# Optimization experiments

Hardware: AMD Instinct MI355X
Metric: run time of the kernel (lower is better)

The kernel has to match this reference:

```python
import jax, jax.numpy as jnp
import numpy as np

NUM_HEADS = 8
T = 8  # hardcoded temporal dim in the original forward
MD = 3  # max_displacement -> 7x7 window
EPS = 1e-12  # F.normalize eps


def l2_normalize(x, axis):
    n = jnp.sqrt(jnp.sum(x * x, axis=axis, keepdims=True))
    return x / jnp.maximum(n, EPS)


def correlation_7x7(q, k):
    # q, k: [B, C, H, W]; FlowNet-style correlation, kernel_size=1, max_disp=3.
    # out[b, u, v, h, w] = sum_c q[b,c,h,w] * k[b,c,h+u-3,w+v-3] (zero padded)
    B, C, H, W = q.shape
    kp = jnp.pad(k, ((0, 0), (0, 0), (MD, MD), (MD, MD)))
    outs = []
    for dy in range(2 * MD + 1):
        for dx in range(2 * MD + 1):
            ks = kp[:, :, dy:dy + H, dx:dx + W]
            outs.append(jnp.sum(q * ks, axis=1))  # [B, H, W]
    corr = jnp.stack(outs, axis=1)  # [B, 49, H, W]
    return corr.reshape(B, 2 * MD + 1, 2 * MD + 1, H, W)


def setup_inputs() -> dict:
    key = jax.random.key(0)
    ks = jax.random.split(key, 6)
    B, N, C = 8, 8192, 256
    hd = C // NUM_HEADS
    std = 0.02
    return {
        "x": jax.random.normal(ks[0], (B, N, C), dtype=jnp.float32),
        "w_qk": jax.random.normal(ks[1], (2 * C, C), dtype=jnp.float32) * std,
        "w_corr": jax.random.normal(ks[2], (hd, 49), dtype=jnp.float32) * std,
        "b_corr": jnp.zeros((hd,), dtype=jnp.float32),
        "w_proj": jax.random.normal(ks[3], (C, C), dtype=jnp.float32) * std,
        "b_proj": jnp.zeros((C,), dtype=jnp.float32),
    }


def reference(x, w_qk, w_corr, b_corr, w_proj, b_proj):
    B, N, C = x.shape
    nh = NUM_HEADS
    hd = C // nh
    H = int(np.sqrt(N // T))
    W = H

    # qk projection (no bias): [B, N, 2C] -> q, k each [B, nh, N, hd]
    qk = jnp.einsum('bnc,dc->bnd', x, w_qk)
    qk = qk.reshape(B, N, 2, nh, hd).transpose(2, 0, 3, 1, 4)
    q, k = qk[0], qk[1]

    # 'b n (t h w) d -> (b n) t d h w'
    q = q.reshape(B * nh, T, H, W, hd).transpose(0, 1, 4, 2, 3)
    k = k.reshape(B * nh, T, H, W, hd).transpose(0, 1, 4, 2, 3)

    # temporal postfix: k[t+1], last frame repeated
    k_post = jnp.concatenate([k[:, 1:], k[:, -1:]], axis=1)

    qp = q.reshape(B * nh * T, hd, H, W)
    kp = k_post.reshape(B * nh * T, hd, H, W)
    qp = l2_normalize(qp, axis=1)
    kp = l2_normalize(kp, axis=1)

    corr = correlation_7x7(qp, kp)  # [(B nh T), 7, 7, H, W]
    # 'b u v h w -> b (h w) (u v)'
    corr = corr.transpose(0, 3, 4, 1, 2).reshape(B * nh * T, H * W, 49)

    v = jnp.einsum('bpk,dk->bpd', corr, w_corr) + b_corr  # [(B nh T), HW, hd]

    # '(b n t) (h w) d -> b n (t h w) d' then 'b h n d -> b n (h d)'
    out = v.reshape(B, nh, T * H * W, hd).transpose(0, 2, 1, 3).reshape(B, N, C)
    out = jnp.einsum('bnc,dc->bnd', out, w_proj) + b_proj
    return out
```

## Files before the change

### kernel.cpp

```cpp
#include <hip/hip_runtime.h>

typedef _Float16 half8 __attribute__((ext_vector_type(8)));
typedef _Float16 half2v __attribute__((ext_vector_type(2)));
typedef float float4v __attribute__((ext_vector_type(4)));

__device__ __forceinline__ float dot2acc(unsigned a, unsigned b, float c) {
#if __has_builtin(__builtin_amdgcn_fdot2)
  return __builtin_amdgcn_fdot2(__builtin_bit_cast(half2v, a), __builtin_bit_cast(half2v, b), c, false);
#else
  half2v ha = __builtin_bit_cast(half2v, a);
  half2v hb = __builtin_bit_cast(half2v, b);
  c += (float)ha[0] * (float)hb[0];
  c += (float)ha[1] * (float)hb[1];
  return c;
#endif
}
__device__ __forceinline__ unsigned hscale(unsigned a, float s) {
  half2v ha = __builtin_bit_cast(half2v, a);
  half2v r;
  r[0] = (_Float16)((float)ha[0] * s);
  r[1] = (_Float16)((float)ha[1] * s);
  return __builtin_bit_cast(unsigned, r);
}
__device__ __forceinline__ void gload_lds16(const void* g, void* l) {
  __builtin_amdgcn_global_load_lds((const __attribute__((address_space(1))) unsigned*)g,
                                   (__attribute__((address_space(3))) unsigned*)l, 16, 0, 0);
}

__global__ void cvt_all(const float4* __restrict__ x, const float4* __restrict__ wqk,
                        const float4* __restrict__ wpj,
                        ushort4* __restrict__ x16, ushort4* __restrict__ wqk16,
                        ushort4* __restrict__ wpj16) {
  int b = blockIdx.x;
  const float4* s;
  ushort4* d;
  int i;
  if (b < 16384) { s = x; d = x16; i = b * 256 + threadIdx.x; }
  else if (b < 16512) { s = wqk; d = wqk16; i = (b - 16384) * 256 + threadIdx.x; }
  else { s = wpj; d = wpj16; i = (b - 16512) * 256 + threadIdx.x; }
  float4 v = s[i];
  _Float16 a = (_Float16)v.x, bb = (_Float16)v.y, c = (_Float16)v.z, e = (_Float16)v.w;
  ushort4 o;
  o.x = __builtin_bit_cast(unsigned short, a);
  o.y = __builtin_bit_cast(unsigned short, bb);
  o.z = __builtin_bit_cast(unsigned short, c);
  o.w = __builtin_bit_cast(unsigned short, e);
  d[i] = o;
}

__global__ __launch_bounds__(256, 2)
void gemm_qk(const _Float16* __restrict__ A, const _Float16* __restrict__ Bw,
             _Float16* __restrict__ qo, _Float16* __restrict__ ko) {
  __shared__ _Float16 Ash[4096];
  __shared__ _Float16 Bsh[4096];
  const int tid = threadIdx.x;
  const int lane = tid & 63, w = tid >> 6;
  const int wm = w >> 1, wn = w & 1;
  const int ml = lane & 15, qd = lane >> 4;
  const int m0 = blockIdx.y * 128, n0 = blockIdx.x * 128;

  float4v acc[4][4];
  float4v z = {0.f, 0.f, 0.f, 0.f};
#pragma unroll
  for (int i = 0; i < 4; ++i)
#pragma unroll
    for (int j = 0; j < 4; ++j) acc[i][j] = z;

  const _Float16* Ap = A + (size_t)m0 * 256;
  const _Float16* Bp = Bw + (size_t)n0 * 256;
  const int gr = w * 64 + lane;
  const int row0 = gr >> 2, kb = gr & 3;

  for (int kt = 0; kt < 8; ++kt) {
    int k0 = kt * 32;
    gload_lds16(Ap + row0 * 256 + k0 + kb * 8, Ash + (size_t)(w * 64) * 8);
    gload_lds16(Ap + (row0 + 64) * 256 + k0 + kb * 8, Ash + (size_t)(256 + w * 64) * 8);
    gload_lds16(Bp + row0 * 256 + k0 + kb * 8, Bsh + (size_t)(w * 64) * 8);
    gload_lds16(Bp + (row0 + 64) * 256 + k0 + kb * 8, Bsh + (size_t)(256 + w * 64) * 8);
    __syncthreads();
    half8 af[4], bf[4];
#pragma unroll
    for (int im = 0; im < 4; ++im) {
      af[im] = *(const half8*)(Ash + (wm * 64 + im * 16 + ml) * 32 + qd * 8);
      bf[im] = *(const half8*)(Bsh + (wn * 64 + im * 16 + ml) * 32 + qd * 8);
    }
#pragma unroll
    for (int im = 0; im < 4; ++im)
#pragma unroll
      for (int in = 0; in < 4; ++in)
        acc[im][in] = __builtin_amdgcn_mfma_f32_16x16x32_f16(af[im], bf[in], acc[im][in], 0, 0, 0);
    __syncthreads();
  }

#pragma unroll
  for (int im = 0; im < 4; ++im) {
    int rowr0 = m0 + wm * 64 + im * 16 + qd * 4;
#pragma unroll
    for (int in = 0; in < 4; ++in) {
      int col = n0 + wn * 64 + in * 16 + ml;
      int s = col >> 8, h = (col >> 5) & 7, j = col & 31;
      _Float16* dst = s ? ko : qo;
#pragma unroll
      for (int r = 0; r < 4; ++r) {
        int rowr = rowr0 + r;
        int b = rowr >> 13, n = rowr & 8191;
        int t = n >> 10, yx = n & 1023;
        int p = b * 64 + h * 8 + t;
        dst[((size_t)p * 1024 + yx) * 32 + j] = (_Float16)acc[im][in][r];
      }
    }
  }
}

__global__ __launch_bounds__(256, 2)
void corr_kernel(const _Float16* __restrict__ q16, const _Float16* __restrict__ k16,
                 const float* __restrict__ wcorr, const float* __restrict__ bcorr,
                 _Float16* __restrict__ outp) {
  __shared__ __align__(16) _Float16 S[38400];
  _Float16* kt = S;
  _Float16* corrh = S + 15488;
  _Float16* wch = S + 35968;
  constexpr int DUMP = 22528;

  const int tid = threadIdx.x;
  const int bx = blockIdx.x;
  const int p = bx >> 2, tile = bx & 3;
  const int y0 = (tile >> 1) * 16, x0 = (tile & 1) * 16;
  const int b = p >> 6, h = (p >> 3) & 7, t = p & 7;
  const int pk = (t < 7) ? p + 1 : p;

  const int lane = tid & 63, w = tid >> 6;
  const int ml = lane & 15, qd = lane >> 4;

  const _Float16* qbase = q16 + (size_t)p * 32768;
  half8 afrag[4];
#pragma unroll
  for (int yi = 0; yi < 4; ++yi) {
    int yy = 4 * w + yi;
    afrag[yi] = *(const half8*)(qbase + ((size_t)(y0 + yy) * 32 + (x0 + ml)) * 32 + qd * 8);
  }

  for (int idx = tid; idx < 2048; idx += 256) {
    int d = idx >> 6, kk = idx & 63;
    float v = (kk < 49) ? wcorr[d * 49 + kk] : (kk == 49 ? bcorr[d] : 0.f);
    wch[idx] = (_Float16)v;
  }

  const _Float16* kbase = k16 + (size_t)pk * 32768;
#pragma unroll
  for (int i = 0; i < 8; ++i) {
    int g = tid + i * 256;
    if (g < 1936) {
      int vec = g >> 2, part = g & 3;
      int ky = vec / 22, kx = vec - ky * 22;
      int gy = y0 + ky - 3, gx = x0 + kx - 3;
      uint4 val = make_uint4(0u, 0u, 0u, 0u);
      if (gy >= 0 && gy < 32 && gx >= 0 && gx < 32)
        val = *(const uint4*)(kbase + ((size_t)gy * 32 + gx) * 32 + part * 8);
      *(uint4*)(kt + (size_t)g * 8) = val;
    }
  }

#pragma unroll
  for (int yi = 0; yi < 4; ++yi) {
    unsigned* au = (unsigned*)&afrag[yi];
    float ss = 0.f;
#pragma unroll
    for (int e = 0; e < 4; ++e) ss = dot2acc(au[e], au[e], ss);
    ss += __shfl_xor(ss, 16);
    ss += __shfl_xor(ss, 32);
    float sc = 1.f / fmaxf(sqrtf(ss), 1e-12f);
#pragma unroll
    for (int e = 0; e < 4; ++e) au[e] = hscale(au[e], sc);
  }

  {
    uint4 pat = make_uint4(0x3C000000u, 0u, 0u, 0u);
    uint4 zz = make_uint4(0u, 0u, 0u, 0u);
    *(uint4*)(corrh + (size_t)tid * 80 + 48) = pat;
    *(uint4*)(corrh + (size_t)tid * 80 + 56) = zz;
  }

  __syncthreads();

#pragma unroll
  for (int i = 0; i < 8; ++i) {
    int g = tid + i * 256;
    if (g < 1936) {
      uint4 val = *(const uint4*)(kt + (size_t)g * 8);
      unsigned* u = (unsigned*)&val;
      float ss = 0.f;
#pragma unroll
      for (int e = 0; e < 4; ++e) ss = dot2acc(u[e], u[e], ss);
      ss += __shfl_xor(ss, 1);
      ss += __shfl_xor(ss, 2);
      float sc = 1.f / fmaxf(sqrtf(ss), 1e-12f);
#pragma unroll
      for (int e = 0; e < 4; ++e) u[e] = hscale(u[e], sc);
      *(uint4*)(kt + (size_t)g * 8) = val;
    }
  }
  __syncthreads();

  const int bdx = ml - 4 * qd;
  const int lanebase = 5120 * w + 320 * qd + bdx;
  float4v z = {0.f, 0.f, 0.f, 0.f};
#pragma unroll
  for (int kri = 0; kri < 10; ++kri) {
    int kr = 4 * w + kri;
    half8 bf0 = *(const half8*)(kt + ((size_t)kr * 22 + ml) * 32 + qd * 8);
    half8 bf1 = *(const half8*)(kt + ((size_t)kr * 22 + 16 + ml) * 32 + qd * 8);
#pragma unroll
    for (int yi = 0; yi < 4; ++yi) {
      int dy = kri - yi;
      if (dy < 0 || dy > 6) continue;
      float4v r0 = __builtin_amdgcn_mfma_f32_16x16x32_f16(afrag[yi], bf0, z, 0, 0, 0);
      float4v r1 = __builtin_amdgcn_mfma_f32_16x16x32_f16(afrag[yi], bf1, z, 0, 0, 0);
#pragma unroll
      for (int nt = 0; nt < 2; ++nt)
#pragma unroll
        for (int r = 0; r < 4; ++r) {
          int dx = bdx + (16 * nt - r);
          bool ok = (unsigned)dx <= 6u;
          int idx = lanebase + (1280 * yi + 7 * dy + 79 * r + 16 * nt);
          int off = ok ? idx : (DUMP + lane);
          corrh[off] = (_Float16)((nt ? r1 : r0)[r]);
        }
    }
  }
  __syncthreads();

  float4v vacc[4][2];
#pragma unroll
  for (int im = 0; im < 4; ++im) { vacc[im][0] = z; vacc[im][1] = z; }
#pragma unroll
  for (int ks = 0; ks < 2; ++ks) {
    half8 bfrag[2];
#pragma unroll
    for (int nt = 0; nt < 2; ++nt)
      bfrag[nt] = *(const half8*)(wch + (nt * 16 + ml) * 64 + ks * 32 + qd * 8);
#pragma unroll
    for (int im = 0; im < 4; ++im) {
      half8 afr = *(const half8*)(corrh + (size_t)(w * 64 + im * 16 + ml) * 80 + ks * 32 + qd * 8);
#pragma unroll
      for (int nt = 0; nt < 2; ++nt)
        vacc[im][nt] = __builtin_amdgcn_mfma_f32_16x16x32_f16(afr, bfrag[nt], vacc[im][nt], 0, 0, 0);
    }
  }

#pragma unroll
  for (int im = 0; im < 4; ++im) {
#pragma unroll
    for (int nt = 0; nt < 2; ++nt) {
      int d = nt * 16 + ml;
#pragma unroll
      for (int r = 0; r < 4; ++r) {
        int pos = w * 64 + im * 16 + qd * 4 + r;
        int py = pos >> 4, px = pos & 15;
        int n = t * 1024 + (y0 + py) * 32 + (x0 + px);
        outp[(((size_t)b * 8192 + n) << 8) + h * 32 + d] = (_Float16)vacc[im][nt][r];
      }
    }
  }
}

__global__ __launch_bounds__(256, 2)
void gemm_proj(const _Float16* __restrict__ A, const _Float16* __restrict__ Bw,
               const float* __restrict__ bp, float* __restrict__ out) {
  __shared__ _Float16 Ash[4096];
  __shared__ _Float16 Bsh[4096];
  const int tid = threadIdx.x;
  const int lane = tid & 63, w = tid >> 6;
  const int wm = w >> 1, wn = w & 1;
  const int ml = lane & 15, qd = lane >> 4;
  const int m0 = blockIdx.y * 128, n0 = blockIdx.x * 128;

  float4v acc[4][4];
  float4v z = {0.f, 0.f, 0.f, 0.f};
#pragma unroll
  for (int i = 0; i < 4; ++i)
#pragma unroll
    for (int j = 0; j < 4; ++j) acc[i][j] = z;

  const _Float16* Ap = A + (size_t)m0 * 256;
  const _Float16* Bp = Bw + (size_t)n0 * 256;
  const int gr = w * 64 + lane;
  const int row0 = gr >> 2, kb = gr & 3;

  for (int kt = 0; kt < 8; ++kt) {
    int k0 = kt * 32;
    gload_lds16(Ap + row0 * 256 + k0 + kb * 8, Ash + (size_t)(w * 64) * 8);
    gload_lds16(Ap + (row0 + 64) * 256 + k0 + kb * 8, Ash + (size_t)(256 + w * 64) * 8);
    gload_lds16(Bp + row0 * 256 + k0 + kb * 8, Bsh + (size_t)(w * 64) * 8);
    gload_lds16(Bp + (row0 + 64) * 256 + k0 + kb * 8, Bsh + (size_t)(256 + w * 64) * 8);
    __syncthreads();
    half8 af[4], bf[4];
#pragma unroll
    for (int im = 0; im < 4; ++im) {
      af[im] = *(const half8*)(Ash + (wm * 64 + im * 16 + ml) * 32 + qd * 8);
      bf[im] = *(const half8*)(Bsh + (wn * 64 + im * 16 + ml) * 32 + qd * 8);
    }
#pragma unroll
    for (int im = 0; im < 4; ++im)
#pragma unroll
      for (int in = 0; in < 4; ++in)
        acc[im][in] = __builtin_amdgcn_mfma_f32_16x16x32_f16(af[im], bf[in], acc[im][in], 0, 0, 0);
    __syncthreads();
  }

#pragma unroll
  for (int im = 0; im < 4; ++im) {
    int rowr0 = m0 + wm * 64 + im * 16 + qd * 4;
#pragma unroll
    for (int in = 0; in < 4; ++in) {
      int col = n0 + wn * 64 + in * 16 + ml;
      float bias = bp[col];
#pragma unroll
      for (int r = 0; r < 4; ++r)
        out[(size_t)(rowr0 + r) * 256 + col] = acc[im][in][r] + bias;
    }
  }
}

extern "C" void kernel_launch(void* const* d_in, const int* in_sizes, int n_in,
                              void* d_out, int out_size, void* d_ws, size_t ws_size,
                              hipStream_t stream) {
  const float* x      = (const float*)d_in[0];
  const float* w_qk   = (const float*)d_in[1];
  const float* w_corr = (const float*)d_in[2];
  const float* b_corr = (const float*)d_in[3];
  const float* w_proj = (const float*)d_in[4];
  const float* b_proj = (const float*)d_in[5];
  float* out = (float*)d_out;

  char* ws = (char*)d_ws;
  _Float16* x16   = (_Float16*)(ws);
  _Float16* q16   = (_Float16*)(ws + 33554432);
  _Float16* k16   = (_Float16*)(ws + 67108864);
  _Float16* op16  = (_Float16*)(ws + 100663296);
  _Float16* wqk16 = (_Float16*)(ws + 134217728);
  _Float16* wpj16 = (_Float16*)(ws + 134479872);

  cvt_all<<<16576, 256, 0, stream>>>((const float4*)x, (const float4*)w_qk, (const float4*)w_proj,
                                     (ushort4*)x16, (ushort4*)wqk16, (ushort4*)wpj16);
  gemm_qk<<<dim3(4, 512), 256, 0, stream>>>(x16, wqk16, q16, k16);
  corr_kernel<<<2048, 256, 0, stream>>>(q16, k16, w_corr, b_corr, op16);
  gemm_proj<<<dim3(2, 512), 256, 0, stream>>>(op16, wpj16, b_proj, out);
}
```

Before: 244.1 us.

## Restructure corr kernel: direct K loads, swizzled corr layout, staged vectorized output

The correlation kernel no longer stages a padded K tile in LDS. Each wave loads and normalizes its K rows straight from global memory, and the MFMA operands are swapped so results land in a new swizzled 8x16-per-dy corr layout written with packed 64-bit stores. The second GEMM reads shifted dwords to form fragments, adds bias in the epilogue instead of through a padded ones column, and stages outputs in LDS so each thread writes 64 contiguous bytes. This removes the K staging pass, two barriers and the scattered per-element half stores. In exchange it adds redundant K loads and normalization across waves, plus more complex index arithmetic.

```diff
diff --git a/kernel.cpp b/kernel.cpp
--- a/kernel.cpp
+++ b/kernel.cpp
@@ -21,6 +21,12 @@
   r[0] = (_Float16)((float)ha[0] * s);
   r[1] = (_Float16)((float)ha[1] * s);
   return __builtin_bit_cast(unsigned, r);
+}
+__device__ __forceinline__ unsigned pack2(float a, float b) {
+  half2v h;
+  h[0] = (_Float16)a;
+  h[1] = (_Float16)b;
+  return __builtin_bit_cast(unsigned, h);
 }
 __device__ __forceinline__ void gload_lds16(const void* g, void* l) {
   __builtin_amdgcn_global_load_lds((const __attribute__((address_space(1))) unsigned*)g,
@@ -116,11 +122,9 @@
 void corr_kernel(const _Float16* __restrict__ q16, const _Float16* __restrict__ k16,
                  const float* __restrict__ wcorr, const float* __restrict__ bcorr,
                  _Float16* __restrict__ outp) {
-  __shared__ __align__(16) _Float16 S[38400];
-  _Float16* kt = S;
-  _Float16* corrh = S + 15488;
-  _Float16* wch = S + 35968;
-  constexpr int DUMP = 22528;
+  __shared__ __align__(16) _Float16 S[37120];
+  _Float16* corr = S;
+  _Float16* wch = S + 34816;
 
   const int tid = threadIdx.x;
   const int bx = blockIdx.x;
@@ -128,139 +132,192 @@
   const int y0 = (tile >> 1) * 16, x0 = (tile & 1) * 16;
   const int b = p >> 6, h = (p >> 3) & 7, t = p & 7;
   const int pk = (t < 7) ? p + 1 : p;
-
   const int lane = tid & 63, w = tid >> 6;
   const int ml = lane & 15, qd = lane >> 4;
 
+  {
+    int d = tid >> 3, c8 = tid & 7;
+#pragma unroll
+    for (int i = 0; i < 9; ++i) {
+      int kp = c8 * 9 + i;
+      int dy = kp >> 3, dx = kp & 7;
+      float v = (dy < 7 && dx < 7) ? wcorr[d * 49 + dy * 7 + dx] : 0.f;
+      wch[d * 72 + kp] = (_Float16)v;
+    }
+  }
+  {
+    int dyp = 7 ^ ((tid >> 4) & 7);
+    *(uint4*)(corr + tid * 136 + dyp * 16) = make_uint4(0u, 0u, 0u, 0u);
+    *(uint4*)(corr + tid * 136 + dyp * 16 + 8) = make_uint4(0u, 0u, 0u, 0u);
+  }
+
   const _Float16* qbase = q16 + (size_t)p * 32768;
-  half8 afrag[4];
+  half8 qB[4];
 #pragma unroll
   for (int yi = 0; yi < 4; ++yi) {
-    int yy = 4 * w + yi;
-    afrag[yi] = *(const half8*)(qbase + ((size_t)(y0 + yy) * 32 + (x0 + ml)) * 32 + qd * 8);
-  }
-
-  for (int idx = tid; idx < 2048; idx += 256) {
-    int d = idx >> 6, kk = idx & 63;
-    float v = (kk < 49) ? wcorr[d * 49 + kk] : (kk == 49 ? bcorr[d] : 0.f);
-    wch[idx] = (_Float16)v;
-  }
-
-  const _Float16* kbase = k16 + (size_t)pk * 32768;
-#pragma unroll
-  for (int i = 0; i < 8; ++i) {
-    int g = tid + i * 256;
-    if (g < 1936) {
-      int vec = g >> 2, part = g & 3;
-      int ky = vec / 22, kx = vec - ky * 22;
-      int gy = y0 + ky - 3, gx = x0 + kx - 3;
-      uint4 val = make_uint4(0u, 0u, 0u, 0u);
-      if (gy >= 0 && gy < 32 && gx >= 0 && gx < 32)
-        val = *(const uint4*)(kbase + ((size_t)gy * 32 + gx) * 32 + part * 8);
-      *(uint4*)(kt + (size_t)g * 8) = val;
-    }
-  }
-
-#pragma unroll
-  for (int yi = 0; yi < 4; ++yi) {
-    unsigned* au = (unsigned*)&afrag[yi];
+    int y = 4 * w + yi;
+    qB[yi] = *(const half8*)(qbase + (size_t)((y0 + y) * 32 + (x0 + ml)) * 32 + qd * 8);
+    unsigned* u = (unsigned*)&qB[yi];
     float ss = 0.f;
 #pragma unroll
-    for (int e = 0; e < 4; ++e) ss = dot2acc(au[e], au[e], ss);
+    for (int e = 0; e < 4; ++e) ss = dot2acc(u[e], u[e], ss);
     ss += __shfl_xor(ss, 16);
     ss += __shfl_xor(ss, 32);
     float sc = 1.f / fmaxf(sqrtf(ss), 1e-12f);
 #pragma unroll
-    for (int e = 0; e < 4; ++e) au[e] = hscale(au[e], sc);
-  }
-
-  {
-    uint4 pat = make_uint4(0x3C000000u, 0u, 0u, 0u);
-    uint4 zz = make_uint4(0u, 0u, 0u, 0u);
-    *(uint4*)(corrh + (size_t)tid * 80 + 48) = pat;
-    *(uint4*)(corrh + (size_t)tid * 80 + 56) = zz;
-  }
-
-  __syncthreads();
-
-#pragma unroll
-  for (int i = 0; i < 8; ++i) {
-    int g = tid + i * 256;
-    if (g < 1936) {
-      uint4 val = *(const uint4*)(kt + (size_t)g * 8);
-      unsigned* u = (unsigned*)&val;
-      float ss = 0.f;
-#pragma unroll
-      for (int e = 0; e < 4; ++e) ss = dot2acc(u[e], u[e], ss);
-      ss += __shfl_xor(ss, 1);
-      ss += __shfl_xor(ss, 2);
-      float sc = 1.f / fmaxf(sqrtf(ss), 1e-12f);
-#pragma unroll
-      for (int e = 0; e < 4; ++e) u[e] = hscale(u[e], sc);
-      *(uint4*)(kt + (size_t)g * 8) = val;
-    }
-  }
-  __syncthreads();
-
-  const int bdx = ml - 4 * qd;
-  const int lanebase = 5120 * w + 320 * qd + bdx;
-  float4v z = {0.f, 0.f, 0.f, 0.f};
+    for (int e = 0; e < 4; ++e) u[e] = hscale(u[e], sc);
+  }
+
+  const _Float16* kbase = k16 + (size_t)pk * 32768;
+  const float4v zf = {0.f, 0.f, 0.f, 0.f};
+  const int gxa = x0 + ml - 3;
+  const int gxb = gxa + 16;
+  const int cxa = min(max(gxa, 0), 31);
+  const int cxb = min(gxb, 31);
+  const bool vca = (gxa >= 0) && (gxa < 32);
+  const bool vcb = (gxb < 32);
+  const int sx8 = (ml >> 3) << 3;
+  const bool v0 = (ml < 8) || (qd >= 2);
+  const bool v1 = (ml >= 8) && (qd < 2);
+  const int off0 = ((4 * qd) - ((ml >= 8) ? 8 : 0)) ^ sx8;
+  const int off1 = (8 + 4 * qd) ^ sx8;
+
 #pragma unroll
   for (int kri = 0; kri < 10; ++kri) {
-    int kr = 4 * w + kri;
-    half8 bf0 = *(const half8*)(kt + ((size_t)kr * 22 + ml) * 32 + qd * 8);
-    half8 bf1 = *(const half8*)(kt + ((size_t)kr * 22 + 16 + ml) * 32 + qd * 8);
+    int kr = 4 * w - 3 + kri;
+    int gy = y0 + kr;
+    half8 ka0 = {}, kb0 = {};
+    if (gy >= 0 && gy < 32) {
+      ka0 = *(const half8*)(kbase + (size_t)(gy * 32 + cxa) * 32 + qd * 8);
+      kb0 = *(const half8*)(kbase + (size_t)(gy * 32 + cxb) * 32 + qd * 8);
+      {
+        unsigned* u = (unsigned*)&ka0;
+        float ss = 0.f;
+#pragma unroll
+        for (int e = 0; e < 4; ++e) ss = dot2acc(u[e], u[e], ss);
+        ss += __shfl_xor(ss, 16);
+        ss += __shfl_xor(ss, 32);
+        float sc = vca ? 1.f / fmaxf(sqrtf(ss), 1e-12f) : 0.f;
+#pragma unroll
+        for (int e = 0; e < 4; ++e) u[e] = hscale(u[e], sc);
+      }
+      {
+        unsigned* u = (unsigned*)&kb0;
+        float ss = 0.f;
+#pragma unroll
+        for (int e = 0; e < 4; ++e) ss = dot2acc(u[e], u[e], ss);
+        ss += __shfl_xor(ss, 16);
+        ss += __shfl_xor(ss, 32);
+        float sc = vcb ? 1.f / fmaxf(sqrtf(ss), 1e-12f) : 0.f;
+#pragma unroll
+        for (int e = 0; e < 4; ++e) u[e] = hscale(u[e], sc);
+      }
+    }
 #pragma unroll
     for (int yi = 0; yi < 4; ++yi) {
       int dy = kri - yi;
       if (dy < 0 || dy > 6) continue;
-      float4v r0 = __builtin_amdgcn_mfma_f32_16x16x32_f16(afrag[yi], bf0, z, 0, 0, 0);
-      float4v r1 = __builtin_amdgcn_mfma_f32_16x16x32_f16(afrag[yi], bf1, z, 0, 0, 0);
-#pragma unroll
-      for (int nt = 0; nt < 2; ++nt)
-#pragma unroll
-        for (int r = 0; r < 4; ++r) {
-          int dx = bdx + (16 * nt - r);
-          bool ok = (unsigned)dx <= 6u;
-          int idx = lanebase + (1280 * yi + 7 * dy + 79 * r + 16 * nt);
-          int off = ok ? idx : (DUMP + lane);
-          corrh[off] = (_Float16)((nt ? r1 : r0)[r]);
-        }
+      float4v D0 = __builtin_amdgcn_mfma_f32_16x16x32_f16(ka0, qB[yi], zf, 0, 0, 0);
+      float4v D1 = __builtin_amdgcn_mfma_f32_16x16x32_f16(kb0, qB[yi], zf, 0, 0, 0);
+      int y = 4 * w + yi;
+      int base = (16 * ml + y) * 136 + (dy ^ (ml & 7)) * 16;
+      if (v0) {
+        uint2 pk0;
+        pk0.x = pack2(D0[0], D0[1]);
+        pk0.y = pack2(D0[2], D0[3]);
+        *(uint2*)(corr + base + off0) = pk0;
+      }
+      if (v1) {
+        uint2 pk1;
+        pk1.x = pack2(D1[0], D1[1]);
+        pk1.y = pack2(D1[2], D1[3]);
+        *(uint2*)(corr + base + off1) = pk1;
+      }
     }
   }
   __syncthreads();
 
+  half8 wA[2][2];
+#pragma unroll
+  for (int dt = 0; dt < 2; ++dt)
+#pragma unroll
+    for (int ks = 0; ks < 2; ++ks)
+      wA[dt][ks] = *(const half8*)(wch + (dt * 16 + ml) * 72 + ks * 32 + qd * 8);
+
   float4v vacc[4][2];
 #pragma unroll
-  for (int im = 0; im < 4; ++im) { vacc[im][0] = z; vacc[im][1] = z; }
-#pragma unroll
-  for (int ks = 0; ks < 2; ++ks) {
-    half8 bfrag[2];
-#pragma unroll
-    for (int nt = 0; nt < 2; ++nt)
-      bfrag[nt] = *(const half8*)(wch + (nt * 16 + ml) * 64 + ks * 32 + qd * 8);
-#pragma unroll
-    for (int im = 0; im < 4; ++im) {
-      half8 afr = *(const half8*)(corrh + (size_t)(w * 64 + im * 16 + ml) * 80 + ks * 32 + qd * 8);
-#pragma unroll
-      for (int nt = 0; nt < 2; ++nt)
-        vacc[im][nt] = __builtin_amdgcn_mfma_f32_16x16x32_f16(afr, bfrag[nt], vacc[im][nt], 0, 0, 0);
-    }
-  }
-
-#pragma unroll
-  for (int im = 0; im < 4; ++im) {
-#pragma unroll
-    for (int nt = 0; nt < 2; ++nt) {
-      int d = nt * 16 + ml;
-#pragma unroll
-      for (int r = 0; r < 4; ++r) {
-        int pos = w * 64 + im * 16 + qd * 4 + r;
-        int py = pos >> 4, px = pos & 15;
-        int n = t * 1024 + (y0 + py) * 32 + (x0 + px);
-        outp[(((size_t)b * 8192 + n) << 8) + h * 32 + d] = (_Float16)vacc[im][nt][r];
-      }
-    }
+  for (int i = 0; i < 4; ++i) {
+    vacc[i][0] = zf;
+    vacc[i][1] = zf;
+  }
+#pragma unroll
+  for (int i = 0; i < 4; ++i) {
+    int xc = 4 * w + i;
+    int key = xc & 7;
+    int x4 = (xc >> 3) << 2;
+    int e = key >> 1;
+    int sh = key & 1;
+#pragma unroll
+    for (int ks = 0; ks < 2; ++ks) {
+      int dyp = (ks * 4 + qd) ^ key;
+      int base = (16 * xc + ml) * 136 + dyp * 16;
+      unsigned dw[5];
+#pragma unroll
+      for (int tt = 0; tt < 5; ++tt)
+        dw[tt] = *(const unsigned*)(corr + base + (((e + tt) ^ x4) << 1));
+      uint4 bfw;
+      if (sh) {
+        bfw.x = (dw[0] >> 16) | (dw[1] << 16);
+        bfw.y = (dw[1] >> 16) | (dw[2] << 16);
+        bfw.z = (dw[2] >> 16) | (dw[3] << 16);
+        bfw.w = (dw[3] >> 16) | (dw[4] << 16);
+      } else {
+        bfw.x = dw[0]; bfw.y = dw[1]; bfw.z = dw[2]; bfw.w = dw[3];
+      }
+      half8 bfrag = __builtin_bit_cast(half8, bfw);
+#pragma unroll
+      for (int dt = 0; dt < 2; ++dt)
+        vacc[i][dt] = __builtin_amdgcn_mfma_f32_16x16x32_f16(wA[dt][ks], bfrag, vacc[i][dt], 0, 0, 0);
+    }
+  }
+  __syncthreads();
+
+  _Float16* vout = S;
+#pragma unroll
+  for (int i = 0; i < 4; ++i) {
+    int xc = 4 * w + i;
+    int posN = ml * 16 + xc;
+#pragma unroll
+    for (int dt = 0; dt < 2; ++dt) {
+      int d0 = dt * 16 + 4 * qd;
+      float4 bb = *(const float4*)(bcorr + d0);
+      uint2 pkv;
+      pkv.x = pack2(vacc[i][dt][0] + bb.x, vacc[i][dt][1] + bb.y);
+      pkv.y = pack2(vacc[i][dt][2] + bb.z, vacc[i][dt][3] + bb.w);
+      *(uint2*)(vout + posN * 40 + (d0 ^ ((ml & 7) << 2))) = pkv;
+    }
+  }
+  __syncthreads();
+
+  {
+    int key2 = (tid >> 4) & 7;
+    uint2 vv[8];
+#pragma unroll
+    for (int lb = 0; lb < 8; ++lb)
+      vv[lb] = *(const uint2*)(vout + tid * 40 + (((lb ^ key2) << 2)));
+    int y = tid >> 4, x = tid & 15;
+    int n = t * 1024 + (y0 + y) * 32 + (x0 + x);
+    _Float16* dst = outp + (((size_t)(b * 8192 + n)) << 8) + h * 32;
+    uint4 o0, o1;
+    o0.x = vv[0].x; o0.y = vv[0].y; o0.z = vv[1].x; o0.w = vv[1].y;
+    o1.x = vv[2].x; o1.y = vv[2].y; o1.z = vv[3].x; o1.w = vv[3].y;
+    *(uint4*)(dst) = o0;
+    *(uint4*)(dst + 8) = o1;
+    uint4 o2, o3;
+    o2.x = vv[4].x; o2.y = vv[4].y; o2.z = vv[5].x; o2.w = vv[5].y;
+    o3.x = vv[6].x; o3.y = vv[6].y; o3.z = vv[7].x; o3.w = vv[7].y;
+    *(uint4*)(dst + 16) = o2;
+    *(uint4*)(dst + 24) = o3;
   }
 }
 
```

Measured after the change: 245.5 us. Within noise of the previous version (+0.6%).
